# Kernel optimization log

Hardware: AMD Instinct MI355X
Metric: run time of the kernel (lower is better)

## Reference

```python
import jax, jax.numpy as jnp
import numpy as np

N = 8192
D = 128
DEG = 32
E = N * DEG
A = 64


def setup_inputs() -> dict:
    key = jax.random.key(0)
    ks = jax.random.split(key, 10)
    node_features = jax.random.normal(ks[0], (N, D), dtype=jnp.float32)
    edge_features = jax.random.normal(ks[1], (N, N), dtype=jnp.float32)
    # deterministic edge list (distinct (src,dst) pairs, consistent with an adjacency nonzero())
    src_idx = jnp.repeat(jnp.arange(N, dtype=jnp.int32), DEG)
    offs = (jnp.arange(DEG, dtype=jnp.int32) + 1) * 37  # 37*32 < N -> all offsets distinct mod N
    dst_idx = (src_idx + jnp.tile(offs, N)) % N
    # message MLP: Linear(2D+1 -> D)
    W_msg = jax.random.normal(ks[2], (D, 2 * D + 1), dtype=jnp.float32) / np.sqrt(2 * D + 1)
    b_msg = jax.random.normal(ks[3], (D,), dtype=jnp.float32) * 0.01
    # GRUCell(D, D): gates ordered r, z, n
    w_ih = jax.random.normal(ks[4], (3 * D, D), dtype=jnp.float32) / np.sqrt(D)
    w_hh = jax.random.normal(ks[5], (3 * D, D), dtype=jnp.float32) / np.sqrt(D)
    b_ih = jax.random.normal(ks[6], (3 * D,), dtype=jnp.float32) * 0.01
    b_hh = jax.random.normal(ks[7], (3 * D,), dtype=jnp.float32) * 0.01
    # policy readout
    W_pol = jax.random.normal(ks[8], (A, D), dtype=jnp.float32) / np.sqrt(D)
    b_pol = jax.random.normal(ks[9], (A,), dtype=jnp.float32) * 0.01
    return {"node_features": node_features, "edge_features": edge_features,
            "src_idx": src_idx, "dst_idx": dst_idx,
            "W_msg": W_msg, "b_msg": b_msg,
            "w_ih": w_ih, "w_hh": w_hh, "b_ih": b_ih, "b_hh": b_hh,
            "W_pol": W_pol, "b_pol": b_pol}


def reference(node_features, edge_features, src_idx, dst_idx,
              W_msg, b_msg, w_ih, w_hh, b_ih, b_hh, W_pol, b_pol):
    # NOTE: the source loop never reassigns node_features, so every iteration
    # computes the same updated_node_features; we mirror it literally.
    for _ in range(3):
        src = node_features[src_idx]                              # [E, D]
        dst = node_features[dst_idx]                              # [E, D]
        ef = edge_features[src_idx, dst_idx][:, None]             # [E, 1]
        combined = jnp.concatenate([src, dst, ef], axis=1)        # [E, 2D+1]
        messages = jax.nn.relu(combined @ W_msg.T + b_msg)        # [E, D]
        agg = jnp.zeros_like(node_features).at[dst_idx].add(messages)  # [N, D]
        # GRUCell(agg, node_features), torch gate order r, z, n
        gi = agg @ w_ih.T + b_ih                                  # [N, 3D]
        gh = node_features @ w_hh.T + b_hh                        # [N, 3D]
        i_r, i_z, i_n = jnp.split(gi, 3, axis=1)
        h_r, h_z, h_n = jnp.split(gh, 3, axis=1)
        r = jax.nn.sigmoid(i_r + h_r)
        z = jax.nn.sigmoid(i_z + h_z)
        n = jnp.tanh(i_n + r * h_n)
        updated = (1.0 - z) * n + z * node_features               # [N, D]
    node_sum = updated.sum(axis=0)                                # [D]
    return node_sum @ W_pol.T + b_pol                             # [A]
```

## Files before the change

### kernel.cpp

```cpp
#include <hip/hip_runtime.h>

#define NN 8192
#define DD 128
#define DEG 32
#define EE (NN*DEG)
#define AA 64

using short8 = __attribute__((ext_vector_type(8))) short;
using f32x4  = __attribute__((ext_vector_type(4))) float;

__device__ __forceinline__ unsigned short f2bf(float x) {
    unsigned u = __builtin_bit_cast(unsigned, x);
    u += 0x7FFFu + ((u >> 16) & 1u);
    return (unsigned short)(u >> 16);
}
__device__ __forceinline__ float bf2f(unsigned short h) {
    unsigned u = ((unsigned)h) << 16;
    return __builtin_bit_cast(float, u);
}


__global__ __launch_bounds__(256) void prep_kernel(
    const float* __restrict__ nf, const int* __restrict__ src_idx,
    const int* __restrict__ dst_idx,
    const float* __restrict__ W_msg, const float* __restrict__ w_ih,
    const float* __restrict__ w_hh,
    int* __restrict__ inv_src, unsigned short* __restrict__ nfbf,
    float* __restrict__ node_sum, float* __restrict__ w3f,
    unsigned short* __restrict__ W1bf, unsigned short* __restrict__ W2bf,
    unsigned short* __restrict__ wibf, unsigned short* __restrict__ whbf)
{
    const int idx = blockIdx.x * 256 + threadIdx.x;
    {
        int d = dst_idx[idx];
        inv_src[d * DEG + (idx & 31)] = src_idx[idx];
    }
    {
        const float4 v = *(const float4*)&nf[(size_t)idx * 4];
        unsigned short h[4] = { f2bf(v.x), f2bf(v.y), f2bf(v.z), f2bf(v.w) };
        *(uint2*)&nfbf[(size_t)idx * 4] = *(uint2*)h;
    }
    if (idx < DD * DD) {
        int f = idx >> 7, k = idx & 127;
        W1bf[idx] = f2bf(W_msg[f * 257 + k]);
        W2bf[idx] = f2bf(W_msg[f * 257 + 128 + k]);
    }
    if (idx < 384 * DD) {
        wibf[idx] = f2bf(w_ih[idx]);
        whbf[idx] = f2bf(w_hh[idx]);
    }
    if (idx < DD) {
        node_sum[idx] = 0.f;
        w3f[idx] = W_msg[idx * 257 + 256];
    }
}

__global__ __launch_bounds__(128) void pq_gemm_kernel(
    const unsigned short* __restrict__ nfbf,
    const unsigned short* __restrict__ W1bf, const unsigned short* __restrict__ W2bf,
    const float* __restrict__ b_msg,
    float* __restrict__ P, float* __restrict__ Q)
{
    const int t = threadIdx.x;
    const int w = t >> 6, l = t & 63, p = l & 15, q = l >> 4;
    const int rowbase = blockIdx.x * 64 + w * 32;

    f32x4 accP[2][8], accQ[2][8];
    const f32x4 z4 = {0.f, 0.f, 0.f, 0.f};
#pragma unroll
    for (int m = 0; m < 2; ++m)
#pragma unroll
        for (int n = 0; n < 8; ++n) { accP[m][n] = z4; accQ[m][n] = z4; }

#pragma unroll
    for (int ks = 0; ks < 4; ++ks) {
        short8 a0 = *(const short8*)&nfbf[(size_t)(rowbase + p) * DD + ks * 32 + q * 8];
        short8 a1 = *(const short8*)&nfbf[(size_t)(rowbase + 16 + p) * DD + ks * 32 + q * 8];
#pragma unroll
        for (int n = 0; n < 8; ++n) {
            short8 b1 = *(const short8*)&W1bf[(n * 16 + p) * DD + ks * 32 + q * 8];
            short8 b2 = *(const short8*)&W2bf[(n * 16 + p) * DD + ks * 32 + q * 8];
            accP[0][n] = __builtin_amdgcn_mfma_f32_16x16x32_bf16(a0, b1, accP[0][n], 0, 0, 0);
            accP[1][n] = __builtin_amdgcn_mfma_f32_16x16x32_bf16(a1, b1, accP[1][n], 0, 0, 0);
            accQ[0][n] = __builtin_amdgcn_mfma_f32_16x16x32_bf16(a0, b2, accQ[0][n], 0, 0, 0);
            accQ[1][n] = __builtin_amdgcn_mfma_f32_16x16x32_bf16(a1, b2, accQ[1][n], 0, 0, 0);
        }
    }
#pragma unroll
    for (int n = 0; n < 8; ++n) {
        const int col = n * 16 + p;
        const float bv = b_msg[col];
#pragma unroll
        for (int m = 0; m < 2; ++m)
#pragma unroll
            for (int r = 0; r < 4; ++r) {
                const size_t row = rowbase + m * 16 + q * 4 + r;
                P[row * DD + col] = accP[m][n][r];
                Q[row * DD + col] = accQ[m][n][r] + bv;
            }
    }
}

__global__ __launch_bounds__(256) void agg_kernel(
    const float* __restrict__ P, const float* __restrict__ Q,
    const float* __restrict__ efeat, const int* __restrict__ inv_src,
    const float* __restrict__ w3f, unsigned short* __restrict__ aggbf)
{
    __shared__ int   s_src[2][DEG];
    __shared__ float s_ef[2][DEG];
    const int t = threadIdx.x;
    const int blk = blockIdx.x;

    if (t < 64) {
        const int dl = t >> 5, j = t & 31;
        const int d = blk * 2 + dl;
        const int s = inv_src[d * DEG + j];
        s_src[dl][j] = s;
        s_ef[dl][j] = efeat[(size_t)s * NN + d];
    }
    __syncthreads();

    const int dl = t >> 7;
    const int f = t & 127;
    const int d = blk * 2 + dl;
    const float base = Q[(size_t)d * DD + f];
    const float w3v = w3f[f];

    float acc = 0.f;
#pragma unroll
    for (int j = 0; j < DEG; ++j) {
        const int s = s_src[dl][j];
        const float v = P[(size_t)s * DD + f] + base + s_ef[dl][j] * w3v;
        acc += fmaxf(v, 0.f);
    }
    aggbf[(size_t)d * DD + f] = f2bf(acc);
}

__global__ __launch_bounds__(384) void gru_kernel(
    const unsigned short* __restrict__ nfbf, const unsigned short* __restrict__ aggbf,
    const unsigned short* __restrict__ wibf, const unsigned short* __restrict__ whbf,
    const float* __restrict__ b_ih, const float* __restrict__ b_hh,
    float* __restrict__ node_sum)
{
    __shared__ float gate_s[6][32][132];
    const int t = threadIdx.x;
    const int n0 = blockIdx.x * 32;
    const int wv = t >> 6, l = t & 63, p = l & 15, q = l >> 4;
    const unsigned short* Wb = (wv < 3) ? wibf : whbf;
    const unsigned short* Ab = (wv < 3) ? aggbf : nfbf;
    const int rowbase = (wv % 3) * 128;

    f32x4 acc[2][8];
    const f32x4 z4 = {0.f, 0.f, 0.f, 0.f};
#pragma unroll
    for (int n = 0; n < 8; ++n) { acc[0][n] = z4; acc[1][n] = z4; }

#pragma unroll
    for (int ks = 0; ks < 4; ++ks) {
        short8 a0 = *(const short8*)&Ab[(size_t)(n0 + p) * DD + ks * 32 + q * 8];
        short8 a1 = *(const short8*)&Ab[(size_t)(n0 + 16 + p) * DD + ks * 32 + q * 8];
#pragma unroll
        for (int n = 0; n < 8; ++n) {
            short8 b = *(const short8*)&Wb[(size_t)(rowbase + n * 16 + p) * DD + ks * 32 + q * 8];
            acc[0][n] = __builtin_amdgcn_mfma_f32_16x16x32_bf16(a0, b, acc[0][n], 0, 0, 0);
            acc[1][n] = __builtin_amdgcn_mfma_f32_16x16x32_bf16(a1, b, acc[1][n], 0, 0, 0);
        }
    }
#pragma unroll
    for (int n = 0; n < 8; ++n)
#pragma unroll
        for (int m = 0; m < 2; ++m)
#pragma unroll
            for (int r = 0; r < 4; ++r)
                gate_s[wv][m * 16 + q * 4 + r][n * 16 + p] = acc[m][n][r];
    __syncthreads();

    const int f = t & 127;
    const int g3 = t >> 7;
    const float bir = b_ih[f], biz = b_ih[128 + f], bin = b_ih[256 + f];
    const float bhr = b_hh[f], bhz = b_hh[128 + f], bhn = b_hh[256 + f];
    float uloc = 0.f;
    for (int j = g3; j < 32; j += 3) {
        const float ir = gate_s[0][j][f], iz = gate_s[1][j][f], inn = gate_s[2][j][f];
        const float hr = gate_s[3][j][f], hz = gate_s[4][j][f], hn = gate_s[5][j][f];
        const float h = bf2f(nfbf[(size_t)(n0 + j) * DD + f]);
        const float r = 1.f / (1.f + expf(-(ir + bir + hr + bhr)));
        const float z = 1.f / (1.f + expf(-(iz + biz + hz + bhz)));
        const float n = tanhf(inn + bin + r * (hn + bhn));
        uloc += (1.f - z) * n + z * h;
    }
    atomicAdd(&node_sum[f], uloc);
}

__global__ void policy_kernel(const float* __restrict__ node_sum,
                              const float* __restrict__ W_pol,
                              const float* __restrict__ b_pol,
                              float* __restrict__ out)
{
    int a = threadIdx.x;
    if (a < AA) {
        float s = b_pol[a];
        for (int k = 0; k < DD; ++k) s += node_sum[k] * W_pol[a * DD + k];
        out[a] = s;
    }
}

extern "C" void kernel_launch(void* const* d_in, const int* in_sizes, int n_in,
                              void* d_out, int out_size, void* d_ws, size_t ws_size,
                              hipStream_t stream)
{
    const float* nf    = (const float*)d_in[0];
    const float* efeat = (const float*)d_in[1];
    const int*   src   = (const int*)d_in[2];
    const int*   dst   = (const int*)d_in[3];
    const float* W_msg = (const float*)d_in[4];
    const float* b_msg = (const float*)d_in[5];
    const float* w_ih  = (const float*)d_in[6];
    const float* w_hh  = (const float*)d_in[7];
    const float* b_ih  = (const float*)d_in[8];
    const float* b_hh  = (const float*)d_in[9];
    const float* W_pol = (const float*)d_in[10];
    const float* b_pol = (const float*)d_in[11];
    float* out = (float*)d_out;

    char* ws = (char*)d_ws;
    int*            inv_src  = (int*)(ws + 0);
    unsigned short* nfbf     = (unsigned short*)(ws + 1048576);
    unsigned short* aggbf    = (unsigned short*)(ws + 3145728);
    float*          node_sum = (float*)(ws + 5242880);
    float*          w3f      = (float*)(ws + 5243392);
    unsigned short* W1bf     = (unsigned short*)(ws + 5243904);
    unsigned short* W2bf     = (unsigned short*)(ws + 5276672);
    unsigned short* wibf     = (unsigned short*)(ws + 5309440);
    unsigned short* whbf     = (unsigned short*)(ws + 5407744);
    float*          P        = (float*)(ws + 5506048);
    float*          Q        = (float*)(ws + 9700352);

    prep_kernel<<<EE / 256, 256, 0, stream>>>(nf, src, dst, W_msg, w_ih, w_hh,
                                              inv_src, nfbf, node_sum, w3f,
                                              W1bf, W2bf, wibf, whbf);
    pq_gemm_kernel<<<128, 128, 0, stream>>>(nfbf, W1bf, W2bf, b_msg, P, Q);
    agg_kernel<<<NN / 2, 256, 0, stream>>>(P, Q, efeat, inv_src, w3f, aggbf);
    gru_kernel<<<NN / 32, 384, 0, stream>>>(nfbf, aggbf, wibf, whbf,
                                            b_ih, b_hh, node_sum);
    policy_kernel<<<1, 64, 0, stream>>>(node_sum, W_pol, b_pol, out);
}
```

Measured before the change: 72.38 us.

## Fuse all stages into one cooperative persistent kernel with grid syncs

Replaces five separate kernel launches with a single cooperative kernel of 256 blocks by 512 threads, separating the phases with grid.sync. The aim is to remove per-launch overhead and gaps between kernels. The restructure also gathers edge features into a per-destination array during prep, vectorises the aggregation with float4 loads, and fuses the GRU input and hidden GEMMs so gates are computed in registers rather than staged through shared memory. The cost is grid-wide barrier latency, much less parallelism in the small GEMM phases, and the occupancy limits a cooperative launch imposes.

```diff
diff --git a/kernel.cpp b/kernel.cpp
--- a/kernel.cpp
+++ b/kernel.cpp
@@ -1,10 +1,16 @@
 #include <hip/hip_runtime.h>
+#include <hip/hip_cooperative_groups.h>
+
+namespace cg = cooperative_groups;
 
 #define NN 8192
 #define DD 128
 #define DEG 32
 #define EE (NN*DEG)
 #define AA 64
+#define NB 256
+#define NT 512
+#define GSZ (NB*NT)
 
 using short8 = __attribute__((ext_vector_type(8))) short;
 using f32x4  = __attribute__((ext_vector_type(4))) float;
@@ -20,188 +26,188 @@
 }
 
 
-__global__ __launch_bounds__(256) void prep_kernel(
-    const float* __restrict__ nf, const int* __restrict__ src_idx,
-    const int* __restrict__ dst_idx,
-    const float* __restrict__ W_msg, const float* __restrict__ w_ih,
-    const float* __restrict__ w_hh,
-    int* __restrict__ inv_src, unsigned short* __restrict__ nfbf,
-    float* __restrict__ node_sum, float* __restrict__ w3f,
-    unsigned short* __restrict__ W1bf, unsigned short* __restrict__ W2bf,
-    unsigned short* __restrict__ wibf, unsigned short* __restrict__ whbf)
+__global__ __launch_bounds__(NT) void mega_kernel(
+    const float* __restrict__ nf, const float* __restrict__ efeat,
+    const int* __restrict__ src_idx, const int* __restrict__ dst_idx,
+    const float* __restrict__ W_msg, const float* __restrict__ b_msg,
+    const float* __restrict__ w_ih, const float* __restrict__ w_hh,
+    const float* __restrict__ b_ih, const float* __restrict__ b_hh,
+    const float* __restrict__ W_pol, const float* __restrict__ b_pol,
+    float* __restrict__ out, char* __restrict__ ws)
 {
-    const int idx = blockIdx.x * 256 + threadIdx.x;
-    {
-        int d = dst_idx[idx];
-        inv_src[d * DEG + (idx & 31)] = src_idx[idx];
-    }
-    {
-        const float4 v = *(const float4*)&nf[(size_t)idx * 4];
-        unsigned short h[4] = { f2bf(v.x), f2bf(v.y), f2bf(v.z), f2bf(v.w) };
-        *(uint2*)&nfbf[(size_t)idx * 4] = *(uint2*)h;
-    }
-    if (idx < DD * DD) {
-        int f = idx >> 7, k = idx & 127;
-        W1bf[idx] = f2bf(W_msg[f * 257 + k]);
-        W2bf[idx] = f2bf(W_msg[f * 257 + 128 + k]);
-    }
-    if (idx < 384 * DD) {
-        wibf[idx] = f2bf(w_ih[idx]);
-        whbf[idx] = f2bf(w_hh[idx]);
-    }
-    if (idx < DD) {
-        node_sum[idx] = 0.f;
-        w3f[idx] = W_msg[idx * 257 + 256];
-    }
-}
-
-__global__ __launch_bounds__(128) void pq_gemm_kernel(
-    const unsigned short* __restrict__ nfbf,
-    const unsigned short* __restrict__ W1bf, const unsigned short* __restrict__ W2bf,
-    const float* __restrict__ b_msg,
-    float* __restrict__ P, float* __restrict__ Q)
-{
+    cg::grid_group grid = cg::this_grid();
+
+    int*            inv_src  = (int*)(ws);
+    float*          eft      = (float*)(ws + 1048576);
+    unsigned short* nfbf     = (unsigned short*)(ws + 2097152);
+    unsigned short* aggbf    = (unsigned short*)(ws + 4194304);
+    float*          node_sum = (float*)(ws + 6291456);
+    float*          w3f      = (float*)(ws + 6291968);
+    unsigned short* W1bf     = (unsigned short*)(ws + 6292480);
+    unsigned short* W2bf     = (unsigned short*)(ws + 6325248);
+    unsigned short* wibf     = (unsigned short*)(ws + 6358016);
+    unsigned short* whbf     = (unsigned short*)(ws + 6456320);
+    float*          P        = (float*)(ws + 6554624);
+    float*          Q        = (float*)(ws + 10748928);
+
     const int t = threadIdx.x;
-    const int w = t >> 6, l = t & 63, p = l & 15, q = l >> 4;
-    const int rowbase = blockIdx.x * 64 + w * 32;
-
-    f32x4 accP[2][8], accQ[2][8];
-    const f32x4 z4 = {0.f, 0.f, 0.f, 0.f};
-#pragma unroll
-    for (int m = 0; m < 2; ++m)
-#pragma unroll
-        for (int n = 0; n < 8; ++n) { accP[m][n] = z4; accQ[m][n] = z4; }
-
-#pragma unroll
-    for (int ks = 0; ks < 4; ++ks) {
-        short8 a0 = *(const short8*)&nfbf[(size_t)(rowbase + p) * DD + ks * 32 + q * 8];
-        short8 a1 = *(const short8*)&nfbf[(size_t)(rowbase + 16 + p) * DD + ks * 32 + q * 8];
-#pragma unroll
-        for (int n = 0; n < 8; ++n) {
-            short8 b1 = *(const short8*)&W1bf[(n * 16 + p) * DD + ks * 32 + q * 8];
-            short8 b2 = *(const short8*)&W2bf[(n * 16 + p) * DD + ks * 32 + q * 8];
-            accP[0][n] = __builtin_amdgcn_mfma_f32_16x16x32_bf16(a0, b1, accP[0][n], 0, 0, 0);
-            accP[1][n] = __builtin_amdgcn_mfma_f32_16x16x32_bf16(a1, b1, accP[1][n], 0, 0, 0);
-            accQ[0][n] = __builtin_amdgcn_mfma_f32_16x16x32_bf16(a0, b2, accQ[0][n], 0, 0, 0);
-            accQ[1][n] = __builtin_amdgcn_mfma_f32_16x16x32_bf16(a1, b2, accQ[1][n], 0, 0, 0);
-        }
-    }
-#pragma unroll
-    for (int n = 0; n < 8; ++n) {
-        const int col = n * 16 + p;
-        const float bv = b_msg[col];
+    const int b = blockIdx.x;
+    const int g = b * NT + t;
+
+    __shared__ int   s_src[32][32];
+    __shared__ float s_ef[32][32];
+
+    {
+        const float4* nf4 = (const float4*)nf;
+        for (int u = g; u < NN * DD / 4; u += GSZ) {
+            const float4 v = nf4[u];
+            unsigned short h[4] = { f2bf(v.x), f2bf(v.y), f2bf(v.z), f2bf(v.w) };
+            *(uint2*)&nfbf[(size_t)u * 4] = *(uint2*)h;
+        }
+        for (int e = g; e < EE; e += GSZ) {
+            const int d = dst_idx[e], s = src_idx[e];
+            const int slot = d * DEG + (e & 31);
+            inv_src[slot] = s;
+            eft[slot] = efeat[(size_t)s * NN + d];
+        }
+        if (g < DD * DD) {
+            const int f = g >> 7, k = g & 127;
+            W1bf[g] = f2bf(W_msg[f * 257 + k]);
+            W2bf[g] = f2bf(W_msg[f * 257 + 128 + k]);
+        }
+        if (g < 384 * DD) {
+            wibf[g] = f2bf(w_ih[g]);
+            whbf[g] = f2bf(w_hh[g]);
+        }
+        if (g < DD) { node_sum[g] = 0.f; w3f[g] = W_msg[g * 257 + 256]; }
+    }
+    grid.sync();
+
+    {
+        const int w = t >> 6, l = t & 63, p = l & 15, q = l >> 4;
+        const int rowbase = b * 32;
+        const unsigned short* Wb = (w < 4) ? W1bf : W2bf;
+        const int nt0 = (w & 3) * 2;
+        f32x4 acc[2][2];
+        const f32x4 z4 = {0.f, 0.f, 0.f, 0.f};
+        acc[0][0] = z4; acc[0][1] = z4; acc[1][0] = z4; acc[1][1] = z4;
+#pragma unroll
+        for (int ks = 0; ks < 4; ++ks) {
+            short8 a0 = *(const short8*)&nfbf[(size_t)(rowbase + p) * DD + ks * 32 + q * 8];
+            short8 a1 = *(const short8*)&nfbf[(size_t)(rowbase + 16 + p) * DD + ks * 32 + q * 8];
+#pragma unroll
+            for (int ni = 0; ni < 2; ++ni) {
+                short8 bb = *(const short8*)&Wb[((nt0 + ni) * 16 + p) * DD + ks * 32 + q * 8];
+                acc[0][ni] = __builtin_amdgcn_mfma_f32_16x16x32_bf16(a0, bb, acc[0][ni], 0, 0, 0);
+                acc[1][ni] = __builtin_amdgcn_mfma_f32_16x16x32_bf16(a1, bb, acc[1][ni], 0, 0, 0);
+            }
+        }
+        float* Out = (w < 4) ? P : Q;
+#pragma unroll
+        for (int ni = 0; ni < 2; ++ni) {
+            const int col = (nt0 + ni) * 16 + p;
+            const float bv = (w < 4) ? 0.f : b_msg[col];
+#pragma unroll
+            for (int m = 0; m < 2; ++m)
+#pragma unroll
+                for (int r = 0; r < 4; ++r)
+                    Out[(size_t)(rowbase + m * 16 + q * 4 + r) * DD + col] = acc[m][ni][r] + bv;
+        }
+    }
+    grid.sync();
+
+    {
+        for (int i = t; i < 1024; i += NT) {
+            ((int*)s_src)[i]  = inv_src[b * 1024 + i];
+            ((float*)s_ef)[i] = eft[b * 1024 + i];
+        }
+        __syncthreads();
+        const float4* P4 = (const float4*)P;
+        const float4* Q4 = (const float4*)Q;
+        const int c = t & 31;
+        const float4 w3v = ((const float4*)w3f)[c];
+#pragma unroll
+        for (int pass = 0; pass < 2; ++pass) {
+            const int dl = pass * 16 + (t >> 5);
+            const int d = b * 32 + dl;
+            const float4 qv = Q4[(size_t)d * 32 + c];
+            float ax = 0.f, ay = 0.f, az = 0.f, aw = 0.f;
+#pragma unroll
+            for (int j = 0; j < DEG; ++j) {
+                const int s = s_src[dl][j];
+                const float ef = s_ef[dl][j];
+                const float4 pv = P4[(size_t)s * 32 + c];
+                ax += fmaxf(pv.x + qv.x + ef * w3v.x, 0.f);
+                ay += fmaxf(pv.y + qv.y + ef * w3v.y, 0.f);
+                az += fmaxf(pv.z + qv.z + ef * w3v.z, 0.f);
+                aw += fmaxf(pv.w + qv.w + ef * w3v.w, 0.f);
+            }
+            unsigned short h4[4] = { f2bf(ax), f2bf(ay), f2bf(az), f2bf(aw) };
+            *(uint2*)&aggbf[(size_t)d * DD + c * 4] = *(uint2*)h4;
+        }
+    }
+    grid.sync();
+
+    {
+        const int w = t >> 6, l = t & 63, p = l & 15, q = l >> 4;
+        const int n0 = b * 32;
+        const int col = w * 16 + p;
+        f32x4 aR[2], aZ[2], aIN[2], aHN[2];
+        const f32x4 z4 = {0.f, 0.f, 0.f, 0.f};
+        aR[0] = z4; aR[1] = z4; aZ[0] = z4; aZ[1] = z4;
+        aIN[0] = z4; aIN[1] = z4; aHN[0] = z4; aHN[1] = z4;
+#pragma unroll
+        for (int ks = 0; ks < 4; ++ks) {
+            const int ko = ks * 32 + q * 8;
+            short8 g0 = *(const short8*)&aggbf[(size_t)(n0 + p) * DD + ko];
+            short8 g1 = *(const short8*)&aggbf[(size_t)(n0 + 16 + p) * DD + ko];
+            short8 h0 = *(const short8*)&nfbf[(size_t)(n0 + p) * DD + ko];
+            short8 h1 = *(const short8*)&nfbf[(size_t)(n0 + 16 + p) * DD + ko];
+            short8 wir = *(const short8*)&wibf[(size_t)(col) * DD + ko];
+            short8 whr = *(const short8*)&whbf[(size_t)(col) * DD + ko];
+            short8 wiz = *(const short8*)&wibf[(size_t)(128 + col) * DD + ko];
+            short8 whz = *(const short8*)&whbf[(size_t)(128 + col) * DD + ko];
+            short8 win = *(const short8*)&wibf[(size_t)(256 + col) * DD + ko];
+            short8 whn = *(const short8*)&whbf[(size_t)(256 + col) * DD + ko];
+            aR[0] = __builtin_amdgcn_mfma_f32_16x16x32_bf16(g0, wir, aR[0], 0, 0, 0);
+            aR[0] = __builtin_amdgcn_mfma_f32_16x16x32_bf16(h0, whr, aR[0], 0, 0, 0);
+            aR[1] = __builtin_amdgcn_mfma_f32_16x16x32_bf16(g1, wir, aR[1], 0, 0, 0);
+            aR[1] = __builtin_amdgcn_mfma_f32_16x16x32_bf16(h1, whr, aR[1], 0, 0, 0);
+            aZ[0] = __builtin_amdgcn_mfma_f32_16x16x32_bf16(g0, wiz, aZ[0], 0, 0, 0);
+            aZ[0] = __builtin_amdgcn_mfma_f32_16x16x32_bf16(h0, whz, aZ[0], 0, 0, 0);
+            aZ[1] = __builtin_amdgcn_mfma_f32_16x16x32_bf16(g1, wiz, aZ[1], 0, 0, 0);
+            aZ[1] = __builtin_amdgcn_mfma_f32_16x16x32_bf16(h1, whz, aZ[1], 0, 0, 0);
+            aIN[0] = __builtin_amdgcn_mfma_f32_16x16x32_bf16(g0, win, aIN[0], 0, 0, 0);
+            aIN[1] = __builtin_amdgcn_mfma_f32_16x16x32_bf16(g1, win, aIN[1], 0, 0, 0);
+            aHN[0] = __builtin_amdgcn_mfma_f32_16x16x32_bf16(h0, whn, aHN[0], 0, 0, 0);
+            aHN[1] = __builtin_amdgcn_mfma_f32_16x16x32_bf16(h1, whn, aHN[1], 0, 0, 0);
+        }
+        const float cbr  = b_ih[col] + b_hh[col];
+        const float cbz  = b_ih[128 + col] + b_hh[128 + col];
+        const float cbin = b_ih[256 + col];
+        const float cbhn = b_hh[256 + col];
+        float sumv = 0.f;
 #pragma unroll
         for (int m = 0; m < 2; ++m)
 #pragma unroll
-            for (int r = 0; r < 4; ++r) {
-                const size_t row = rowbase + m * 16 + q * 4 + r;
-                P[row * DD + col] = accP[m][n][r];
-                Q[row * DD + col] = accQ[m][n][r] + bv;
+            for (int rr = 0; rr < 4; ++rr) {
+                const int row = n0 + m * 16 + q * 4 + rr;
+                const float r = 1.f / (1.f + expf(-(aR[m][rr] + cbr)));
+                const float z = 1.f / (1.f + expf(-(aZ[m][rr] + cbz)));
+                const float n = tanhf(aIN[m][rr] + cbin + r * (aHN[m][rr] + cbhn));
+                const float h = bf2f(nfbf[(size_t)row * DD + col]);
+                sumv += (1.f - z) * n + z * h;
             }
-    }
-}
-
-__global__ __launch_bounds__(256) void agg_kernel(
-    const float* __restrict__ P, const float* __restrict__ Q,
-    const float* __restrict__ efeat, const int* __restrict__ inv_src,
-    const float* __restrict__ w3f, unsigned short* __restrict__ aggbf)
-{
-    __shared__ int   s_src[2][DEG];
-    __shared__ float s_ef[2][DEG];
-    const int t = threadIdx.x;
-    const int blk = blockIdx.x;
-
-    if (t < 64) {
-        const int dl = t >> 5, j = t & 31;
-        const int d = blk * 2 + dl;
-        const int s = inv_src[d * DEG + j];
-        s_src[dl][j] = s;
-        s_ef[dl][j] = efeat[(size_t)s * NN + d];
-    }
-    __syncthreads();
-
-    const int dl = t >> 7;
-    const int f = t & 127;
-    const int d = blk * 2 + dl;
-    const float base = Q[(size_t)d * DD + f];
-    const float w3v = w3f[f];
-
-    float acc = 0.f;
-#pragma unroll
-    for (int j = 0; j < DEG; ++j) {
-        const int s = s_src[dl][j];
-        const float v = P[(size_t)s * DD + f] + base + s_ef[dl][j] * w3v;
-        acc += fmaxf(v, 0.f);
-    }
-    aggbf[(size_t)d * DD + f] = f2bf(acc);
-}
-
-__global__ __launch_bounds__(384) void gru_kernel(
-    const unsigned short* __restrict__ nfbf, const unsigned short* __restrict__ aggbf,
-    const unsigned short* __restrict__ wibf, const unsigned short* __restrict__ whbf,
-    const float* __restrict__ b_ih, const float* __restrict__ b_hh,
-    float* __restrict__ node_sum)
-{
-    __shared__ float gate_s[6][32][132];
-    const int t = threadIdx.x;
-    const int n0 = blockIdx.x * 32;
-    const int wv = t >> 6, l = t & 63, p = l & 15, q = l >> 4;
-    const unsigned short* Wb = (wv < 3) ? wibf : whbf;
-    const unsigned short* Ab = (wv < 3) ? aggbf : nfbf;
-    const int rowbase = (wv % 3) * 128;
-
-    f32x4 acc[2][8];
-    const f32x4 z4 = {0.f, 0.f, 0.f, 0.f};
-#pragma unroll
-    for (int n = 0; n < 8; ++n) { acc[0][n] = z4; acc[1][n] = z4; }
-
-#pragma unroll
-    for (int ks = 0; ks < 4; ++ks) {
-        short8 a0 = *(const short8*)&Ab[(size_t)(n0 + p) * DD + ks * 32 + q * 8];
-        short8 a1 = *(const short8*)&Ab[(size_t)(n0 + 16 + p) * DD + ks * 32 + q * 8];
-#pragma unroll
-        for (int n = 0; n < 8; ++n) {
-            short8 b = *(const short8*)&Wb[(size_t)(rowbase + n * 16 + p) * DD + ks * 32 + q * 8];
-            acc[0][n] = __builtin_amdgcn_mfma_f32_16x16x32_bf16(a0, b, acc[0][n], 0, 0, 0);
-            acc[1][n] = __builtin_amdgcn_mfma_f32_16x16x32_bf16(a1, b, acc[1][n], 0, 0, 0);
-        }
-    }
-#pragma unroll
-    for (int n = 0; n < 8; ++n)
-#pragma unroll
-        for (int m = 0; m < 2; ++m)
-#pragma unroll
-            for (int r = 0; r < 4; ++r)
-                gate_s[wv][m * 16 + q * 4 + r][n * 16 + p] = acc[m][n][r];
-    __syncthreads();
-
-    const int f = t & 127;
-    const int g3 = t >> 7;
-    const float bir = b_ih[f], biz = b_ih[128 + f], bin = b_ih[256 + f];
-    const float bhr = b_hh[f], bhz = b_hh[128 + f], bhn = b_hh[256 + f];
-    float uloc = 0.f;
-    for (int j = g3; j < 32; j += 3) {
-        const float ir = gate_s[0][j][f], iz = gate_s[1][j][f], inn = gate_s[2][j][f];
-        const float hr = gate_s[3][j][f], hz = gate_s[4][j][f], hn = gate_s[5][j][f];
-        const float h = bf2f(nfbf[(size_t)(n0 + j) * DD + f]);
-        const float r = 1.f / (1.f + expf(-(ir + bir + hr + bhr)));
-        const float z = 1.f / (1.f + expf(-(iz + biz + hz + bhz)));
-        const float n = tanhf(inn + bin + r * (hn + bhn));
-        uloc += (1.f - z) * n + z * h;
-    }
-    atomicAdd(&node_sum[f], uloc);
-}
-
-__global__ void policy_kernel(const float* __restrict__ node_sum,
-                              const float* __restrict__ W_pol,
-                              const float* __restrict__ b_pol,
-                              float* __restrict__ out)
-{
-    int a = threadIdx.x;
-    if (a < AA) {
-        float s = b_pol[a];
-        for (int k = 0; k < DD; ++k) s += node_sum[k] * W_pol[a * DD + k];
-        out[a] = s;
+        sumv += __shfl_xor(sumv, 16);
+        sumv += __shfl_xor(sumv, 32);
+        if (q == 0) atomicAdd(&node_sum[col], sumv);
+    }
+    grid.sync();
+
+    if (b == 0 && t < AA) {
+        float s = b_pol[t];
+        for (int k = 0; k < DD; ++k) s += node_sum[k] * W_pol[t * DD + k];
+        out[t] = s;
     }
 }
 
@@ -222,26 +228,10 @@
     const float* W_pol = (const float*)d_in[10];
     const float* b_pol = (const float*)d_in[11];
     float* out = (float*)d_out;
-
     char* ws = (char*)d_ws;
-    int*            inv_src  = (int*)(ws + 0);
-    unsigned short* nfbf     = (unsigned short*)(ws + 1048576);
-    unsigned short* aggbf    = (unsigned short*)(ws + 3145728);
-    float*          node_sum = (float*)(ws + 5242880);
-    float*          w3f      = (float*)(ws + 5243392);
-    unsigned short* W1bf     = (unsigned short*)(ws + 5243904);
-    unsigned short* W2bf     = (unsigned short*)(ws + 5276672);
-    unsigned short* wibf     = (unsigned short*)(ws + 5309440);
-    unsigned short* whbf     = (unsigned short*)(ws + 5407744);
-    float*          P        = (float*)(ws + 5506048);
-    float*          Q        = (float*)(ws + 9700352);
-
-    prep_kernel<<<EE / 256, 256, 0, stream>>>(nf, src, dst, W_msg, w_ih, w_hh,
-                                              inv_src, nfbf, node_sum, w3f,
-                                              W1bf, W2bf, wibf, whbf);
-    pq_gemm_kernel<<<128, 128, 0, stream>>>(nfbf, W1bf, W2bf, b_msg, P, Q);
-    agg_kernel<<<NN / 2, 256, 0, stream>>>(P, Q, efeat, inv_src, w3f, aggbf);
-    gru_kernel<<<NN / 32, 384, 0, stream>>>(nfbf, aggbf, wibf, whbf,
-                                            b_ih, b_hh, node_sum);
-    policy_kernel<<<1, 64, 0, stream>>>(node_sum, W_pol, b_pol, out);
-}
+
+    void* args[] = { &nf, &efeat, &src, &dst, &W_msg, &b_msg, &w_ih, &w_hh,
+                     &b_ih, &b_hh, &W_pol, &b_pol, &out, &ws };
+    hipLaunchCooperativeKernel((const void*)mega_kernel, dim3(NB), dim3(NT),
+                               args, 0, stream);
+}
```

Result: slower. 186.1 us (+157.1%).
